# Kernel tuning notes

Measured on AMD Instinct MI355X. Metric: run time of the kernel, lower is better.

Reference implementation:

```python
import jax, jax.numpy as jnp
import numpy as np

N_NODES = 4096
N_EDGES = 65536
N_FEAT = 128
HIDDEN = 64
N_FILT = 8


def setup_inputs() -> dict:
    key = jax.random.key(0)
    k1, k2, k3, k4, k5, k6 = jax.random.split(key, 6)
    X = jax.random.normal(k1, (N_NODES, N_FEAT), dtype=jnp.float32)
    edge_list = jax.random.randint(k2, (2, N_EDGES), 0, N_NODES)
    W1 = jax.random.normal(k3, (N_FEAT, HIDDEN), dtype=jnp.float32) / np.sqrt(N_FEAT)
    b1 = jax.random.normal(k4, (HIDDEN,), dtype=jnp.float32) * 0.01
    W2 = jax.random.normal(k5, (HIDDEN, N_FILT), dtype=jnp.float32) / np.sqrt(HIDDEN)
    b2 = jax.random.normal(k6, (N_FILT,), dtype=jnp.float32) * 0.01
    return {"X": X, "edge_list": edge_list, "W1": W1, "b1": b1, "W2": W2, "b2": b2}


def _diagram0(vals, adj):
    """0-dim persistence of one filtration via incremental union-find.

    Faithful to the torch code: nodes are inserted in ascending filtration
    order; when node v (sorted rank j) is inserted, it is connected to every
    already-present in-neighbor u (edge u->v in edge_list). A component's
    root is its member with minimal rank (what DFS-over-sorted-order picks as
    component[0]). A root born at step b that loses root status at step d has
    longevity (b, d-1); roots alive at the end get (b, inf).
    Returns (pairs [n,2], born_mask [n]) indexed by rank; masked rows are the
    entries the torch dict would contain, in the same (insertion) order.
    """
    n = vals.shape[0]
    order = jnp.argsort(vals)          # node id at each rank
    rank = jnp.argsort(order)          # rank of each node id
    ranks = jnp.arange(n)

    def step(carry, j):
        root, alive, death = carry     # root[node] -> root rank; alive/death indexed by rank
        v = order[j]
        nbr = adj[v] & (rank < j)                      # present in-neighbors of v
        cand = jnp.where(nbr, root, j)                 # roots to merge (j for non-nbrs)
        m = jnp.min(cand)                              # elder root (min rank) of merged comp
        merged = jnp.zeros(n, dtype=bool).at[cand].set(True)
        dies = merged & alive & (ranks != m)           # younger roots die now
        death = jnp.where(dies, (j - 1).astype(jnp.float32), death)
        alive = (alive & ~dies).at[j].set(m == j)      # v is born as a root iff isolated
        root = jnp.where(merged[root], m, root)
        return (root, alive, death), None

    init = (rank, jnp.zeros(n, dtype=bool), jnp.full(n, jnp.inf, dtype=jnp.float32))
    (root, alive, death), _ = jax.lax.scan(step, init, jnp.arange(n))
    born = alive | jnp.isfinite(death)                 # ranks that ever were roots
    pairs = jnp.stack([ranks.astype(jnp.float32), death], axis=1)  # (birth, death)
    return pairs, born


def reference(X, edge_list, W1, b1, W2, b2):
    n = X.shape[0]
    # filtrations = Linear -> ReLU -> Linear
    filt = jnp.maximum(X @ W1 + b1, 0.0) @ W2 + b2     # [n, n_filtrations]
    src, tgt = edge_list[0], edge_list[1]
    adj = jnp.zeros((n, n), dtype=bool).at[tgt, src].set(True)  # adj[v,u]: edge u->v
    pairs, mask = jax.vmap(lambda v: _diagram0(v, adj))(filt.T)
    return pairs, mask  # [F, n, 2] persistence pairs + [F, n] validity mask
```

## Files before the change

### kernel.cpp

```cpp
#include <hip/hip_runtime.h>
#include <hip/hip_bf16.h>
#include <cmath>

static constexpr int NN = 4096;
static constexpr int NE = 65536;
static constexpr int NF = 128;
static constexpr int NH = 64;
static constexpr int NQ = 8;
static constexpr int ECAP = 8192;

static constexpr float DEATH_SENTINEL_F = 3.3895313892515355e38f;

__global__ __launch_bounds__(256) void tg_mlp(const float* __restrict__ X,
                                              const float* __restrict__ W1,
                                              const float* __restrict__ b1,
                                              const float* __restrict__ W2,
                                              const float* __restrict__ b2,
                                              float* __restrict__ filt)
{
    __shared__ float sW1[NF * NH];
    __shared__ float sW2[NH * NQ];
    __shared__ float sb1[NH];
    __shared__ float sb2[NQ];
    const int tid = threadIdx.x;
    for (int i = tid; i < NF * NH; i += 256) sW1[i] = W1[i];
    for (int i = tid; i < NH * NQ; i += 256) sW2[i] = W2[i];
    if (tid < NH) sb1[tid] = b1[tid];
    if (tid < NQ) sb2[tid] = b2[tid];
    __syncthreads();

    const int node = blockIdx.x * 256 + tid;
    const float* xrow = X + (size_t)node * NF;

    double acc[NH];
#pragma unroll
    for (int h = 0; h < NH; ++h) acc[h] = (double)sb1[h];

    for (int k0 = 0; k0 < NF; k0 += 8) {
        float xv[8];
#pragma unroll
        for (int kk = 0; kk < 8; ++kk) xv[kk] = xrow[k0 + kk];
#pragma unroll
        for (int kk = 0; kk < 8; ++kk) {
            const float* wrow = &sW1[(k0 + kk) * NH];
            const double xd = (double)xv[kk];
#pragma unroll
            for (int h = 0; h < NH; ++h) acc[h] += xd * (double)wrow[h];
        }
    }
    double o[NQ];
#pragma unroll
    for (int f = 0; f < NQ; ++f) o[f] = (double)sb2[f];
#pragma unroll
    for (int h = 0; h < NH; ++h) {
        const float hv = fmaxf((float)acc[h], 0.0f);
        const double hd = (double)hv;
#pragma unroll
        for (int f = 0; f < NQ; ++f) o[f] += hd * (double)sW2[h * NQ + f];
    }
#pragma unroll
    for (int f = 0; f < NQ; ++f) filt[node * NQ + f] = (float)o[f];
}

__global__ __launch_bounds__(1024) void tg_sort(const float* __restrict__ filt,
                                                int* __restrict__ rankv)
{
    const int f = blockIdx.x;
    const int tid = threadIdx.x;
    __shared__ float sv[NN];
    __shared__ int   si[NN];
    for (int i = tid; i < NN; i += 1024) { sv[i] = filt[i * NQ + f]; si[i] = i; }
    __syncthreads();
    for (int k = 2; k <= NN; k <<= 1) {
        for (int j = k >> 1; j > 0; j >>= 1) {
            for (int i = tid; i < NN; i += 1024) {
                const int l = i ^ j;
                if (l > i) {
                    const float a = sv[i], b = sv[l];
                    const int ia = si[i], ib = si[l];
                    const bool up = ((i & k) == 0);
                    const bool agtb = (a > b) || (a == b && ia > ib);
                    if (up ? agtb : !agtb) {
                        sv[i] = b; sv[l] = a; si[i] = ib; si[l] = ia;
                    }
                }
            }
            __syncthreads();
        }
    }
    for (int j2 = tid; j2 < NN; j2 += 1024) {
        rankv[f * NN + si[j2]] = j2;
    }
}

__global__ void tg_rzero(int* __restrict__ rdeg, int* __restrict__ rcursor)
{
    const int i = blockIdx.x * 256 + threadIdx.x;
    if (i < NQ * NN) { rdeg[i] = 0; rcursor[i] = 0; }
}

__global__ void tg_rhist(const int* __restrict__ srcn, const int* __restrict__ tgt,
                         const int* __restrict__ rankv, int* __restrict__ rdeg)
{
    const int e = blockIdx.x * 256 + threadIdx.x;
    if (e >= NE) return;
    const int u = srcn[e], v = tgt[e];
#pragma unroll
    for (int f = 0; f < NQ; ++f) {
        const int rs = rankv[f * NN + u];
        const int rt = rankv[f * NN + v];
        if (rs < rt) atomicAdd(&rdeg[f * NN + rt], 1);
    }
}

__global__ __launch_bounds__(1024) void tg_rscan(const int* __restrict__ rdeg, int* __restrict__ rstarts)
{
    const int f = blockIdx.x;
    const int* in = rdeg + f * NN;
    int* outp = rstarts + f * (NN + 1);
    __shared__ int bufA[NN];
    __shared__ int bufB[NN];
    const int tid = threadIdx.x;
    for (int i = tid; i < NN; i += 1024) bufA[i] = in[i];
    __syncthreads();
    int* s = bufA;
    int* d = bufB;
    for (int off = 1; off < NN; off <<= 1) {
        for (int i = tid; i < NN; i += 1024) d[i] = s[i] + ((i >= off) ? s[i - off] : 0);
        __syncthreads();
        int* t = s; s = d; d = t;
    }
    for (int i = tid; i < NN; i += 1024) outp[i + 1] = s[i];
    if (tid == 0) outp[0] = 0;
}

__global__ void tg_rscatter(const int* __restrict__ srcn, const int* __restrict__ tgt,
                            const int* __restrict__ rankv, const int* __restrict__ rstarts,
                            int* __restrict__ rcursor, unsigned short* __restrict__ rcsr16)
{
    const int e = blockIdx.x * 256 + threadIdx.x;
    if (e >= NE) return;
    const int u = srcn[e], v = tgt[e];
#pragma unroll
    for (int f = 0; f < NQ; ++f) {
        const int rs = rankv[f * NN + u];
        const int rt = rankv[f * NN + v];
        if (rs < rt) {
            const int pos = rstarts[f * (NN + 1) + rt] + atomicAdd(&rcursor[f * NN + rt], 1);
            rcsr16[(size_t)f * NE + pos] = (unsigned short)rs;
        }
    }
}

__device__ __forceinline__ int wave_min_i32(int m)
{
    m = min(m, __builtin_amdgcn_update_dpp(0x7fffffff, m, 0x111, 0xF, 0xF, false));
    m = min(m, __builtin_amdgcn_update_dpp(0x7fffffff, m, 0x112, 0xF, 0xF, false));
    m = min(m, __builtin_amdgcn_update_dpp(0x7fffffff, m, 0x114, 0xF, 0xF, false));
    m = min(m, __builtin_amdgcn_update_dpp(0x7fffffff, m, 0x118, 0xF, 0xF, false));
    m = min(m, __builtin_amdgcn_update_dpp(0x7fffffff, m, 0x142, 0xF, 0xF, false));
    m = min(m, __builtin_amdgcn_update_dpp(0x7fffffff, m, 0x143, 0xF, 0xF, false));
    return __builtin_amdgcn_readlane(m, 63);
}

__global__ __launch_bounds__(64) void tg_uf(const int* __restrict__ rstarts,
                                            const unsigned short* __restrict__ rcsr16,
                                            __hip_bfloat16* __restrict__ out)
{
    const int f = blockIdx.x;
    const int lane = threadIdx.x;
    __shared__ int parent[NN];
    __shared__ int death[NN];
    __shared__ unsigned short ebuf[ECAP];

    const unsigned short* grcsr = rcsr16 + (size_t)f * NE;
    const int* rrow = rstarts + f * (NN + 1);

    for (int i = lane; i < NN; i += 64) { parent[i] = i; death[i] = 0x7fffffff; }
    __syncthreads();

    for (int j0 = 0; j0 < NN; j0 += 64) {
        const int rs  = rrow[j0 + lane];
        const int rs2 = rrow[j0 + lane + 1];
        const int deg = rs2 - rs;
        const int s0    = __builtin_amdgcn_readlane(rs, 0);
        const int wend  = __builtin_amdgcn_readlane(rs2, 63);
        const int wcount = wend - s0;

        if (wcount <= ECAP) {
            for (int k = lane; k < wcount; k += 64) ebuf[k] = grcsr[s0 + k];
            __syncthreads();

            for (int k = lane; k < wcount; k += 64) {
                int x = ebuf[k];
                int p = parent[x];
                if (p != x) {
                    int r = p;
                    int q = parent[r];
                    while (q != r) { r = q; q = parent[r]; }
                    parent[x] = r;
                    p = r;
                }
                ebuf[k] = (unsigned short)p;
            }
            __syncthreads();

            int c0 = 0;
            bool interesting = false;
            if (deg > 0) {
                c0 = ebuf[rs - s0];
                bool diff = false;
                for (int b = 1; b < deg; ++b)
                    diff |= ((int)ebuf[rs - s0 + b] != c0);
                interesting = diff;
            }
            if (deg > 0 && !interesting) parent[j0 + lane] = c0;
            __syncthreads();

            unsigned long long imask = __ballot(interesting);
            while (imask) {
                const int jj = __builtin_ctzll(imask);
                imask &= imask - 1;
                const int j  = j0 + jj;
                const int sj = __builtin_amdgcn_readlane(rs, jj);
                const int dj = __builtin_amdgcn_readlane(rs2, jj) - sj;
                int m;
                if (dj <= 64) {
                    int rfin = 0x7fffffff;
                    if (lane < dj) {
                        int x = (int)ebuf[sj - s0 + lane];
                        int p = parent[x];
                        while (p != x) { x = p; p = parent[x]; }
                        rfin = x;
                    }
                    m = wave_min_i32(rfin);
                    if (lane < dj && rfin != m) {
                        death[rfin] = j - 1;
                        parent[rfin] = m;
                    }
                } else {
                    int rmin = 0x7fffffff;
                    for (int b = lane; b < dj; b += 64) {
                        int x = (int)ebuf[sj - s0 + b];
                        int p = parent[x];
                        while (p != x) { x = p; p = parent[x]; }
                        rmin = min(rmin, x);
                    }
                    m = wave_min_i32(rmin);
                    for (int b = lane; b < dj; b += 64) {
                        int x = (int)ebuf[sj - s0 + b];
                        int p = parent[x];
                        while (p != x) { x = p; p = parent[x]; }
                        if (x != m) { death[x] = j - 1; parent[x] = m; }
                    }
                }
                if (lane == 0) parent[j] = m;
            }
            __syncthreads();
        } else {
            for (int jj = 0; jj < 64; ++jj) {
                const int j  = j0 + jj;
                const int sj = __builtin_amdgcn_readlane(rs, jj);
                const int dj = __builtin_amdgcn_readlane(rs2, jj) - sj;
                if (dj == 0) continue;
                int rmin = 0x7fffffff;
                for (int b = lane; b < dj; b += 64) {
                    int x = (int)grcsr[sj + b];
                    int p = parent[x];
                    while (p != x) { x = p; p = parent[x]; }
                    rmin = min(rmin, x);
                }
                const int m = wave_min_i32(rmin);
                for (int b = lane; b < dj; b += 64) {
                    int x = (int)grcsr[sj + b];
                    int p = parent[x];
                    while (p != x) { x = p; p = parent[x]; }
                    if (x != m) { death[x] = j - 1; parent[x] = m; }
                }
                if (lane == 0) parent[j] = m;
                __syncthreads();
            }
        }
    }

    __hip_bfloat16* pairs = out;
    __hip_bfloat16* masko = out + NQ * NN * 2;
    const __hip_bfloat16 bsent = __float2bfloat16(DEATH_SENTINEL_F);
    for (int i = lane; i < NN; i += 64) {
        const int d = death[i];
        const int degi = rrow[i + 1] - rrow[i];
        pairs[(f * NN + i) * 2 + 0] = __float2bfloat16((float)i);
        pairs[(f * NN + i) * 2 + 1] = (d == 0x7fffffff) ? bsent : __float2bfloat16((float)d);
        const bool bornm = (degi == 0) || (d != 0x7fffffff);
        masko[f * NN + i] = __float2bfloat16(bornm ? 1.0f : 0.0f);
    }
}

extern "C" void kernel_launch(void* const* d_in, const int* in_sizes, int n_in,
                              void* d_out, int out_size, void* d_ws, size_t ws_size,
                              hipStream_t stream)
{
    const float* X  = (const float*)d_in[0];
    const int* edges = (const int*)d_in[1];
    const float* W1 = (const float*)d_in[2];
    const float* b1 = (const float*)d_in[3];
    const float* W2 = (const float*)d_in[4];
    const float* b2 = (const float*)d_in[5];
    __hip_bfloat16* out = (__hip_bfloat16*)d_out;

    char* ws = (char*)d_ws;
    float* filt            = (float*)(ws + 0);
    int* rankv             = (int*)(ws + 131072);
    int* rdeg              = (int*)(ws + 262144);
    int* rcursor           = (int*)(ws + 393216);
    int* rstarts           = (int*)(ws + 524288);
    unsigned short* rcsr16 = (unsigned short*)(ws + 655424);

    const int* srcn = edges;
    const int* tgt  = edges + NE;

    tg_mlp<<<NN / 256, 256, 0, stream>>>(X, W1, b1, W2, b2, filt);
    tg_sort<<<NQ, 1024, 0, stream>>>(filt, rankv);
    tg_rzero<<<(NQ * NN) / 256, 256, 0, stream>>>(rdeg, rcursor);
    tg_rhist<<<NE / 256, 256, 0, stream>>>(srcn, tgt, rankv, rdeg);
    tg_rscan<<<NQ, 1024, 0, stream>>>(rdeg, rstarts);
    tg_rscatter<<<NE / 256, 256, 0, stream>>>(srcn, tgt, rankv, rstarts, rcursor, rcsr16);
    tg_uf<<<NQ, 64, 0, stream>>>(rstarts, rcsr16, out);
}
```

Measured before the change: 686.6 us.

## Pipeline union-find across waves: helper waves pre-resolve roots for next window

The union-find kernel moves from one wave to four per filtration. Three helper waves load the next 64-node window's edges from global memory, resolve their roots against the current parent array, and write per-node 'differs' flags into a double buffer. Meanwhile wave 0 applies merges for the previous window, and it now uses path halving. This overlaps global loads and root lookups with the serial merge work. The helpers read parent roots while wave 0 is still merging, so their roots may be stale. That is only safe if the merge path re-resolves every root it uses, which it does for flagged nodes, but unflagged nodes take ebuf's c0 directly, and a stale c0 could be wrong.

```diff
diff --git a/kernel.cpp b/kernel.cpp
--- a/kernel.cpp
+++ b/kernel.cpp
@@ -7,7 +7,7 @@
 static constexpr int NF = 128;
 static constexpr int NH = 64;
 static constexpr int NQ = 8;
-static constexpr int ECAP = 8192;
+static constexpr int ECAP = 4096;
 
 static constexpr float DEATH_SENTINEL_F = 3.3895313892515355e38f;
 
@@ -163,130 +163,130 @@
     return __builtin_amdgcn_readlane(m, 63);
 }
 
-__global__ __launch_bounds__(64) void tg_uf(const int* __restrict__ rstarts,
-                                            const unsigned short* __restrict__ rcsr16,
-                                            __hip_bfloat16* __restrict__ out)
+__global__ __launch_bounds__(256) void tg_uf(const int* __restrict__ rstarts,
+                                             const unsigned short* __restrict__ rcsr16,
+                                             __hip_bfloat16* __restrict__ out)
 {
     const int f = blockIdx.x;
-    const int lane = threadIdx.x;
+    const int t = threadIdx.x;
+    const int lane = t & 63;
+    const int wid = t >> 6;
     __shared__ int parent[NN];
     __shared__ int death[NN];
-    __shared__ unsigned short ebuf[ECAP];
+    __shared__ unsigned short ebuf[2][ECAP];
+    __shared__ unsigned char sflag3[2][3][64];
 
     const unsigned short* grcsr = rcsr16 + (size_t)f * NE;
     const int* rrow = rstarts + f * (NN + 1);
 
-    for (int i = lane; i < NN; i += 64) { parent[i] = i; death[i] = 0x7fffffff; }
+    for (int i = t; i < NN; i += 256) { parent[i] = i; death[i] = 0x7fffffff; }
     __syncthreads();
 
-    for (int j0 = 0; j0 < NN; j0 += 64) {
-        const int rs  = rrow[j0 + lane];
-        const int rs2 = rrow[j0 + lane + 1];
-        const int deg = rs2 - rs;
-        const int s0    = __builtin_amdgcn_readlane(rs, 0);
-        const int wend  = __builtin_amdgcn_readlane(rs2, 63);
-        const int wcount = wend - s0;
-
-        if (wcount <= ECAP) {
-            for (int k = lane; k < wcount; k += 64) ebuf[k] = grcsr[s0 + k];
-            __syncthreads();
-
-            for (int k = lane; k < wcount; k += 64) {
-                int x = ebuf[k];
-                int p = parent[x];
-                if (p != x) {
-                    int r = p;
-                    int q = parent[r];
-                    while (q != r) { r = q; q = parent[r]; }
-                    parent[x] = r;
-                    p = r;
-                }
-                ebuf[k] = (unsigned short)p;
-            }
-            __syncthreads();
-
-            int c0 = 0;
-            bool interesting = false;
-            if (deg > 0) {
-                c0 = ebuf[rs - s0];
-                bool diff = false;
-                for (int b = 1; b < deg; ++b)
-                    diff |= ((int)ebuf[rs - s0 + b] != c0);
-                interesting = diff;
-            }
-            if (deg > 0 && !interesting) parent[j0 + lane] = c0;
-            __syncthreads();
-
-            unsigned long long imask = __ballot(interesting);
-            while (imask) {
-                const int jj = __builtin_ctzll(imask);
-                imask &= imask - 1;
-                const int j  = j0 + jj;
-                const int sj = __builtin_amdgcn_readlane(rs, jj);
-                const int dj = __builtin_amdgcn_readlane(rs2, jj) - sj;
-                int m;
-                if (dj <= 64) {
-                    int rfin = 0x7fffffff;
-                    if (lane < dj) {
-                        int x = (int)ebuf[sj - s0 + lane];
-                        int p = parent[x];
-                        while (p != x) { x = p; p = parent[x]; }
-                        rfin = x;
-                    }
-                    m = wave_min_i32(rfin);
-                    if (lane < dj && rfin != m) {
-                        death[rfin] = j - 1;
-                        parent[rfin] = m;
+    volatile int* vparent = parent;
+
+    for (int it = 0; it <= 64; ++it) {
+        if (wid == 0) {
+            if (it > 0) {
+                const int w  = it - 1;
+                const int j0 = w * 64;
+                const int b  = w & 1;
+                const int rs  = rrow[j0 + lane];
+                const int rs2 = rrow[j0 + lane + 1];
+                const int deg = rs2 - rs;
+                const int s0w    = __shfl(rs, 0);
+                const int wcount = __shfl(rs2, 63) - s0w;
+                if (wcount <= ECAP) {
+                    const int off = rs - s0w;
+                    const bool flag = (deg > 0) &&
+                        ((sflag3[b][0][lane] | sflag3[b][1][lane] | sflag3[b][2][lane]) != 0);
+                    if (deg > 0 && !flag) parent[j0 + lane] = (int)ebuf[b][off];
+                    unsigned long long imask = __ballot(flag);
+                    while (imask) {
+                        const int jj = __builtin_ctzll(imask);
+                        imask &= imask - 1;
+                        const int j   = j0 + jj;
+                        const int sof = __shfl(off, jj);
+                        const int dj  = __shfl(deg, jj);
+                        int rmin = 0x7fffffff;
+                        for (int e = lane; e < dj; e += 64) {
+                            int x = (int)ebuf[b][sof + e];
+                            int p = parent[x];
+                            while (p != x) { const int g = parent[p]; parent[x] = g; x = g; p = parent[x]; }
+                            rmin = min(rmin, x);
+                        }
+                        const int m = wave_min_i32(rmin);
+                        for (int e = lane; e < dj; e += 64) {
+                            int x = (int)ebuf[b][sof + e];
+                            int p = parent[x];
+                            while (p != x) { x = p; p = parent[x]; }
+                            if (x != m) { death[x] = j - 1; parent[x] = m; }
+                        }
+                        if (lane == 0) parent[j] = m;
                     }
                 } else {
-                    int rmin = 0x7fffffff;
-                    for (int b = lane; b < dj; b += 64) {
-                        int x = (int)ebuf[sj - s0 + b];
-                        int p = parent[x];
-                        while (p != x) { x = p; p = parent[x]; }
-                        rmin = min(rmin, x);
-                    }
-                    m = wave_min_i32(rmin);
-                    for (int b = lane; b < dj; b += 64) {
-                        int x = (int)ebuf[sj - s0 + b];
-                        int p = parent[x];
-                        while (p != x) { x = p; p = parent[x]; }
-                        if (x != m) { death[x] = j - 1; parent[x] = m; }
+                    for (int jj = 0; jj < 64; ++jj) {
+                        const int j  = j0 + jj;
+                        const int sj = __shfl(rs, jj);
+                        const int dj = __shfl(deg, jj);
+                        if (dj == 0) continue;
+                        int rmin = 0x7fffffff;
+                        for (int e = lane; e < dj; e += 64) {
+                            int x = (int)grcsr[sj + e];
+                            int p = parent[x];
+                            while (p != x) { const int g = parent[p]; parent[x] = g; x = g; p = parent[x]; }
+                            rmin = min(rmin, x);
+                        }
+                        const int m = wave_min_i32(rmin);
+                        for (int e = lane; e < dj; e += 64) {
+                            int x = (int)grcsr[sj + e];
+                            int p = parent[x];
+                            while (p != x) { x = p; p = parent[x]; }
+                            if (x != m) { death[x] = j - 1; parent[x] = m; }
+                        }
+                        if (lane == 0) parent[j] = m;
                     }
                 }
-                if (lane == 0) parent[j] = m;
             }
-            __syncthreads();
         } else {
-            for (int jj = 0; jj < 64; ++jj) {
-                const int j  = j0 + jj;
-                const int sj = __builtin_amdgcn_readlane(rs, jj);
-                const int dj = __builtin_amdgcn_readlane(rs2, jj) - sj;
-                if (dj == 0) continue;
-                int rmin = 0x7fffffff;
-                for (int b = lane; b < dj; b += 64) {
-                    int x = (int)grcsr[sj + b];
-                    int p = parent[x];
-                    while (p != x) { x = p; p = parent[x]; }
-                    rmin = min(rmin, x);
+            if (it < 64) {
+                const int w    = it;
+                const int j0   = w * 64;
+                const int bb   = w & 1;
+                const int part = wid - 1;
+                const int jj   = lane;
+                const int sA   = rrow[j0 + jj];
+                const int sB   = rrow[j0 + jj + 1];
+                const int s0w  = rrow[j0];
+                const int wcount = rrow[j0 + 64] - s0w;
+                if (wcount <= ECAP) {
+                    const int deg = sB - sA;
+                    const int off = sA - s0w;
+                    bool diff = false;
+                    if (deg > 0) {
+                        int x0 = (int)grcsr[sA];
+                        int p0 = vparent[x0];
+                        while (p0 != x0) { x0 = p0; p0 = vparent[x0]; }
+                        const int c0 = x0;
+                        if (part == 0) ebuf[bb][off] = (unsigned short)c0;
+                        for (int e = (part == 0 ? 3 : part); e < deg; e += 3) {
+                            int x = (int)grcsr[sA + e];
+                            int p = vparent[x];
+                            while (p != x) { x = p; p = vparent[x]; }
+                            ebuf[bb][off + e] = (unsigned short)x;
+                            diff |= (x != c0);
+                        }
+                    }
+                    sflag3[bb][part][jj] = diff ? 1 : 0;
                 }
-                const int m = wave_min_i32(rmin);
-                for (int b = lane; b < dj; b += 64) {
-                    int x = (int)grcsr[sj + b];
-                    int p = parent[x];
-                    while (p != x) { x = p; p = parent[x]; }
-                    if (x != m) { death[x] = j - 1; parent[x] = m; }
-                }
-                if (lane == 0) parent[j] = m;
-                __syncthreads();
             }
         }
+        __syncthreads();
     }
 
     __hip_bfloat16* pairs = out;
     __hip_bfloat16* masko = out + NQ * NN * 2;
     const __hip_bfloat16 bsent = __float2bfloat16(DEATH_SENTINEL_F);
-    for (int i = lane; i < NN; i += 64) {
+    for (int i = t; i < NN; i += 256) {
         const int d = death[i];
         const int degi = rrow[i + 1] - rrow[i];
         pairs[(f * NN + i) * 2 + 0] = __float2bfloat16((float)i);
@@ -325,5 +325,5 @@
     tg_rhist<<<NE / 256, 256, 0, stream>>>(srcn, tgt, rankv, rdeg);
     tg_rscan<<<NQ, 1024, 0, stream>>>(rdeg, rstarts);
     tg_rscatter<<<NE / 256, 256, 0, stream>>>(srcn, tgt, rankv, rstarts, rcursor, rcsr16);
-    tg_uf<<<NQ, 64, 0, stream>>>(rstarts, rcsr16, out);
-}
+    tg_uf<<<NQ, 256, 0, stream>>>(rstarts, rcsr16, out);
+}
```

Result: slower. 717.1 us (+4.4%).
